# Kernel optimization log

Hardware: AMD Instinct MI355X
Metric: run time of the kernel (lower is better)

The kernel has to match this reference:

```python
import jax, jax.numpy as jnp
import numpy as np

IN_DIM, H_DIM, Y_DIM, ROLLOUT = 1024, 2048, 1024, 512


def setup_inputs() -> dict:
    key = jax.random.key(0)
    ks = jax.random.split(key, 4)
    return {
        "x": jax.random.normal(ks[0], (1, ROLLOUT, IN_DIM), dtype=jnp.float32),
        "h": jnp.zeros((H_DIM,), dtype=jnp.float32),
        "Wc": jax.random.normal(ks[1], (IN_DIM + H_DIM, H_DIM), dtype=jnp.float32) * 0.01,
        "Wu": jax.random.normal(ks[2], (IN_DIM + H_DIM, H_DIM), dtype=jnp.float32) * 0.01,
        "bc": jnp.zeros((H_DIM,), dtype=jnp.float32),
        "bu": jnp.zeros((H_DIM,), dtype=jnp.float32),
        "Wh_y": jax.random.normal(ks[3], (H_DIM, Y_DIM), dtype=jnp.float32) * 0.01,
        "by": jnp.zeros((Y_DIM,), dtype=jnp.float32),
    }


def reference(x, h, Wc, Wu, bc, bu, Wh_y, by):
    # x: [1, T, in_dim]; h: [h_dim]. Strict sequential GRU-style cell via scan.
    def step(h_prev, xt):
        xc = jnp.concatenate([xt, h_prev])           # [in+h]
        Lu = jax.nn.sigmoid(xc @ Wu + bu)            # update gate
        c_tilda = jnp.tanh(xc @ Wc + bc)             # candidate
        h_new = Lu * c_tilda + (1.0 - Lu) * h_prev
        y = h_new @ Wh_y + by
        return h_new, y

    h_final, ys = jax.lax.scan(step, h, x[0])        # ys: [T, y_dim]
    return ys, h_final
```

## Files before the change

### kernel.cpp

```cpp
#include <hip/hip_runtime.h>
#include <hip/hip_bf16.h>
#include <math.h>

#define T_STEPS 512
#define IN_DIM  1024
#define H_DIM   2048
#define Y_DIM   1024
#define NBLK    256
#define BTHREADS 512
#define NGRP    8
#define GRP_SZ  (NBLK / NGRP)

static __device__ __forceinline__ unsigned short f2bf(float f) {
    unsigned u = __float_as_uint(f);
    unsigned r = (u + 0x7FFFu + ((u >> 16) & 1u)) >> 16;
    return (unsigned short)r;
}

#define TM 64
#define TN 64
#define TK 16

__global__ __launch_bounds__(256) void gemm_bias(
    const float* __restrict__ A, const float* __restrict__ B,
    const float* __restrict__ bias, float* __restrict__ C,
    int M, int N, int K, int lda, int ldb, int ldc)
{
    __shared__ float As[TK][TM + 4];
    __shared__ float Bs[TK][TN + 4];

    const int n0 = blockIdx.x * TN;
    const int m0 = blockIdx.y * TM;
    const int tid = threadIdx.x;
    const int tx = tid & 15;
    const int ty = tid >> 4;

    float acc[4][4] = {};

    for (int k0 = 0; k0 < K; k0 += TK) {
        #pragma unroll
        for (int l = tid; l < TM * TK; l += 256) {
            int tt = l >> 4, kk = l & 15;
            As[kk][tt] = A[(m0 + tt) * lda + (k0 + kk)];
        }
        #pragma unroll
        for (int l = tid; l < TK * TN; l += 256) {
            int kk = l >> 6, jj = l & 63;
            Bs[kk][jj] = B[(k0 + kk) * ldb + (n0 + jj)];
        }
        __syncthreads();
        #pragma unroll
        for (int kk = 0; kk < TK; ++kk) {
            float4 a = *(const float4*)&As[kk][ty * 4];
            float4 b = *(const float4*)&Bs[kk][tx * 4];
            acc[0][0] = fmaf(a.x, b.x, acc[0][0]);
            acc[0][1] = fmaf(a.x, b.y, acc[0][1]);
            acc[0][2] = fmaf(a.x, b.z, acc[0][2]);
            acc[0][3] = fmaf(a.x, b.w, acc[0][3]);
            acc[1][0] = fmaf(a.y, b.x, acc[1][0]);
            acc[1][1] = fmaf(a.y, b.y, acc[1][1]);
            acc[1][2] = fmaf(a.y, b.z, acc[1][2]);
            acc[1][3] = fmaf(a.y, b.w, acc[1][3]);
            acc[2][0] = fmaf(a.z, b.x, acc[2][0]);
            acc[2][1] = fmaf(a.z, b.y, acc[2][1]);
            acc[2][2] = fmaf(a.z, b.z, acc[2][2]);
            acc[2][3] = fmaf(a.z, b.w, acc[2][3]);
            acc[3][0] = fmaf(a.w, b.x, acc[3][0]);
            acc[3][1] = fmaf(a.w, b.y, acc[3][1]);
            acc[3][2] = fmaf(a.w, b.z, acc[3][2]);
            acc[3][3] = fmaf(a.w, b.w, acc[3][3]);
        }
        __syncthreads();
    }

    float4 bv = *(const float4*)&bias[n0 + tx * 4];
    #pragma unroll
    for (int r = 0; r < 4; ++r) {
        float4 o;
        o.x = acc[r][0] + bv.x;
        o.y = acc[r][1] + bv.y;
        o.z = acc[r][2] + bv.z;
        o.w = acc[r][3] + bv.w;
        *(float4*)&C[(m0 + ty * 4 + r) * ldc + (n0 + tx * 4)] = o;
    }
}

__global__ __launch_bounds__(BTHREADS) void gru_seq(
    const float* __restrict__ Wu_h,
    const float* __restrict__ Wc_h,
    const float* __restrict__ XU,
    const float* __restrict__ XC,
    const float* __restrict__ h0,
    float* __restrict__ H,
    unsigned* __restrict__ bar)
{
    __shared__ unsigned w_lds[2][8][H_DIM / 2];

    const int tid = threadIdx.x;
    const int jb = blockIdx.x * 8;

    for (int idx = tid; idx < 2 * 8 * (H_DIM / 2); idx += BTHREADS) {
        int m = idx >> 13;
        int r = idx & 8191;
        int w = r >> 10;
        int p = r & 1023;
        const float* W = m ? Wc_h : Wu_h;
        int j = jb + w;
        float v0 = W[(2 * p) * H_DIM + j];
        float v1 = W[(2 * p + 1) * H_DIM + j];
        w_lds[m][w][p] = (unsigned)f2bf(v0) | ((unsigned)f2bf(v1) << 16);
    }
    __syncthreads();

    const int w = tid >> 6;
    const int lane = tid & 63;
    const int j = jb + w;
    const unsigned* __restrict__ wu = w_lds[0][w];
    const unsigned* __restrict__ wc = w_lds[1][w];

    unsigned* grp  = bar + (blockIdx.x & (NGRP - 1)) * 64;
    unsigned* root = bar + 512;

    for (int t = 0; t < T_STEPS; ++t) {
        float xu = 0.f, xc = 0.f;
        if (lane == 0) {
            xu = XU[t * H_DIM + j];
            xc = XC[t * H_DIM + j];
        }

        if (t > 0 && tid == 0) {
            unsigned tgt = (unsigned)t * NGRP;
            while (__hip_atomic_load(root, __ATOMIC_RELAXED, __HIP_MEMORY_SCOPE_AGENT) < tgt) {
                __builtin_amdgcn_s_sleep(8);
            }
        }
        __syncthreads();

        const float* hsrc = t ? (H + (t - 1) * H_DIM) : h0;
        const unsigned long long* h64 = (const unsigned long long*)hsrc;

        float hp = 0.f;
        if (lane == 0) {
            hp = __hip_atomic_load((const float*)hsrc + j,
                                   __ATOMIC_RELAXED, __HIP_MEMORY_SCOPE_AGENT);
        }

        float au = 0.f, ac = 0.f;
        #pragma unroll
        for (int i = 0; i < 16; ++i) {
            int p = i * 64 + lane;
            unsigned long long v = __hip_atomic_load(h64 + p,
                                       __ATOMIC_RELAXED, __HIP_MEMORY_SCOPE_AGENT);
            float hx = __uint_as_float((unsigned)v);
            float hy = __uint_as_float((unsigned)(v >> 32));
            unsigned pu = wu[p];
            unsigned pc = wc[p];
            float u0 = __uint_as_float(pu << 16);
            float u1 = __uint_as_float(pu & 0xFFFF0000u);
            float c0 = __uint_as_float(pc << 16);
            float c1 = __uint_as_float(pc & 0xFFFF0000u);
            au = fmaf(hx, u0, au);
            au = fmaf(hy, u1, au);
            ac = fmaf(hx, c0, ac);
            ac = fmaf(hy, c1, ac);
        }
        #pragma unroll
        for (int off = 32; off; off >>= 1) {
            au += __shfl_down(au, off);
            ac += __shfl_down(ac, off);
        }
        if (lane == 0) {
            float pre_u = au + xu;
            float pre_c = ac + xc;
            float ug = 1.f / (1.f + expf(-pre_u));
            float cg = tanhf(pre_c);
            float hnew = ug * cg + (1.f - ug) * hp;
            __hip_atomic_store(H + t * H_DIM + j, hnew,
                               __ATOMIC_RELAXED, __HIP_MEMORY_SCOPE_AGENT);
        }

        asm volatile("s_waitcnt vmcnt(0)" ::: "memory");
        __syncthreads();
        if (tid == 0 && t < T_STEPS - 1) {
            unsigned old = __hip_atomic_fetch_add(grp, 1u,
                               __ATOMIC_RELAXED, __HIP_MEMORY_SCOPE_AGENT);
            if (old == (unsigned)(t + 1) * GRP_SZ - 1u) {
                __hip_atomic_fetch_add(root, 1u,
                                       __ATOMIC_RELAXED, __HIP_MEMORY_SCOPE_AGENT);
            }
        }
    }
}

extern "C" void kernel_launch(void* const* d_in, const int* in_sizes, int n_in,
                              void* d_out, int out_size, void* d_ws, size_t ws_size,
                              hipStream_t stream)
{
    const float* x   = (const float*)d_in[0];
    const float* h0  = (const float*)d_in[1];
    const float* Wc  = (const float*)d_in[2];
    const float* Wu  = (const float*)d_in[3];
    const float* bc  = (const float*)d_in[4];
    const float* bu  = (const float*)d_in[5];
    const float* Why = (const float*)d_in[6];
    const float* by  = (const float*)d_in[7];
    float* out = (float*)d_out;

    float* ws = (float*)d_ws;
    float* XU = ws;
    float* XC = ws + (T_STEPS * H_DIM);
    float* H  = ws + 2 * (T_STEPS * H_DIM);
    unsigned* bar = (unsigned*)(ws + 3 * (T_STEPS * H_DIM));

    hipMemsetAsync(bar, 0, 4096, stream);

    gemm_bias<<<dim3(H_DIM / TN, T_STEPS / TM), 256, 0, stream>>>(
        x, Wu, bu, XU, T_STEPS, H_DIM, IN_DIM, IN_DIM, H_DIM, H_DIM);
    gemm_bias<<<dim3(H_DIM / TN, T_STEPS / TM), 256, 0, stream>>>(
        x, Wc, bc, XC, T_STEPS, H_DIM, IN_DIM, IN_DIM, H_DIM, H_DIM);

    gru_seq<<<NBLK, BTHREADS, 0, stream>>>(
        Wu + IN_DIM * H_DIM, Wc + IN_DIM * H_DIM, XU, XC, h0, H, bar);

    gemm_bias<<<dim3(Y_DIM / TN, T_STEPS / TM), 256, 0, stream>>>(
        H, Why, by, out, T_STEPS, Y_DIM, H_DIM, H_DIM, Y_DIM, Y_DIM);

    hipMemcpyAsync(out + T_STEPS * Y_DIM, H + (T_STEPS - 1) * H_DIM,
                   H_DIM * sizeof(float), hipMemcpyDeviceToDevice, stream);
}
```

Measured before the change: 2.741 ms.

## Halve GRU blocks, keep weights in registers, flatten grid barrier, widen GEMM tiles

The sequential GRU kernel now runs on 128 blocks, each handling 16 hidden units, with each wave computing two units. Recurrent weights are held in registers as packed bf16 rather than in LDS. The two-level group/root barrier is replaced by a single level: eight threads each poll one of eight group counters, with a shorter sleep. This removes the root-counter hop and LDS reads on the per-step critical path. The input and output GEMMs widen the N tile to 128 and use float4 loads. The cost is higher register pressure, 64 weight registers per thread, and more polling traffic.

New measurement: 4.200 ms. +53.3%, slower.

```diff
diff --git a/kernel.cpp b/kernel.cpp
--- a/kernel.cpp
+++ b/kernel.cpp
@@ -6,19 +6,22 @@
 #define IN_DIM  1024
 #define H_DIM   2048
 #define Y_DIM   1024
-#define NBLK    256
-#define BTHREADS 512
-#define NGRP    8
-#define GRP_SZ  (NBLK / NGRP)
+
+#define NBLK2   128
+#define BT2     512
+#define NLINE   8
+#define BLKS_PER_LINE (NBLK2 / NLINE)
 
 static __device__ __forceinline__ unsigned short f2bf(float f) {
     unsigned u = __float_as_uint(f);
     unsigned r = (u + 0x7FFFu + ((u >> 16) & 1u)) >> 16;
     return (unsigned short)r;
 }
+static __device__ __forceinline__ float bflo(unsigned p) { return __uint_as_float(p << 16); }
+static __device__ __forceinline__ float bfhi(unsigned p) { return __uint_as_float(p & 0xFFFF0000u); }
 
 #define TM 64
-#define TN 64
+#define TN 128
 #define TK 16
 
 __global__ __launch_bounds__(256) void gemm_bias(
@@ -35,57 +38,56 @@
     const int tx = tid & 15;
     const int ty = tid >> 4;
 
-    float acc[4][4] = {};
+    float acc[4][8] = {};
 
     for (int k0 = 0; k0 < K; k0 += TK) {
-        #pragma unroll
-        for (int l = tid; l < TM * TK; l += 256) {
-            int tt = l >> 4, kk = l & 15;
-            As[kk][tt] = A[(m0 + tt) * lda + (k0 + kk)];
-        }
-        #pragma unroll
-        for (int l = tid; l < TK * TN; l += 256) {
-            int kk = l >> 6, jj = l & 63;
-            Bs[kk][jj] = B[(k0 + kk) * ldb + (n0 + jj)];
+        {
+            int mm = tid & 63, kq = tid >> 6;
+            float4 a = *(const float4*)&A[(m0 + mm) * lda + k0 + 4 * kq];
+            As[4 * kq + 0][mm] = a.x;
+            As[4 * kq + 1][mm] = a.y;
+            As[4 * kq + 2][mm] = a.z;
+            As[4 * kq + 3][mm] = a.w;
+        }
+        #pragma unroll
+        for (int l = tid; l < 512; l += 256) {
+            int kk = l >> 5, jj = (l & 31) * 4;
+            *(float4*)&Bs[kk][jj] = *(const float4*)&B[(k0 + kk) * ldb + n0 + jj];
         }
         __syncthreads();
         #pragma unroll
         for (int kk = 0; kk < TK; ++kk) {
-            float4 a = *(const float4*)&As[kk][ty * 4];
-            float4 b = *(const float4*)&Bs[kk][tx * 4];
-            acc[0][0] = fmaf(a.x, b.x, acc[0][0]);
-            acc[0][1] = fmaf(a.x, b.y, acc[0][1]);
-            acc[0][2] = fmaf(a.x, b.z, acc[0][2]);
-            acc[0][3] = fmaf(a.x, b.w, acc[0][3]);
-            acc[1][0] = fmaf(a.y, b.x, acc[1][0]);
-            acc[1][1] = fmaf(a.y, b.y, acc[1][1]);
-            acc[1][2] = fmaf(a.y, b.z, acc[1][2]);
-            acc[1][3] = fmaf(a.y, b.w, acc[1][3]);
-            acc[2][0] = fmaf(a.z, b.x, acc[2][0]);
-            acc[2][1] = fmaf(a.z, b.y, acc[2][1]);
-            acc[2][2] = fmaf(a.z, b.z, acc[2][2]);
-            acc[2][3] = fmaf(a.z, b.w, acc[2][3]);
-            acc[3][0] = fmaf(a.w, b.x, acc[3][0]);
-            acc[3][1] = fmaf(a.w, b.y, acc[3][1]);
-            acc[3][2] = fmaf(a.w, b.z, acc[3][2]);
-            acc[3][3] = fmaf(a.w, b.w, acc[3][3]);
+            float4 a  = *(const float4*)&As[kk][ty * 4];
+            float4 b0 = *(const float4*)&Bs[kk][tx * 8];
+            float4 b1 = *(const float4*)&Bs[kk][tx * 8 + 4];
+            const float av[4] = {a.x, a.y, a.z, a.w};
+            const float bv[8] = {b0.x, b0.y, b0.z, b0.w, b1.x, b1.y, b1.z, b1.w};
+            #pragma unroll
+            for (int r = 0; r < 4; ++r)
+                #pragma unroll
+                for (int c = 0; c < 8; ++c)
+                    acc[r][c] = fmaf(av[r], bv[c], acc[r][c]);
         }
         __syncthreads();
     }
 
-    float4 bv = *(const float4*)&bias[n0 + tx * 4];
+    float4 bv0 = *(const float4*)&bias[n0 + tx * 8];
+    float4 bv1 = *(const float4*)&bias[n0 + tx * 8 + 4];
+    const float bb[8] = {bv0.x, bv0.y, bv0.z, bv0.w, bv1.x, bv1.y, bv1.z, bv1.w};
     #pragma unroll
     for (int r = 0; r < 4; ++r) {
-        float4 o;
-        o.x = acc[r][0] + bv.x;
-        o.y = acc[r][1] + bv.y;
-        o.z = acc[r][2] + bv.z;
-        o.w = acc[r][3] + bv.w;
-        *(float4*)&C[(m0 + ty * 4 + r) * ldc + (n0 + tx * 4)] = o;
-    }
-}
-
-__global__ __launch_bounds__(BTHREADS) void gru_seq(
+        float4 o0, o1;
+        o0.x = acc[r][0] + bb[0]; o0.y = acc[r][1] + bb[1];
+        o0.z = acc[r][2] + bb[2]; o0.w = acc[r][3] + bb[3];
+        o1.x = acc[r][4] + bb[4]; o1.y = acc[r][5] + bb[5];
+        o1.z = acc[r][6] + bb[6]; o1.w = acc[r][7] + bb[7];
+        float* cp = &C[(m0 + ty * 4 + r) * ldc + n0 + tx * 8];
+        *(float4*)cp = o0;
+        *(float4*)(cp + 4) = o1;
+    }
+}
+
+__global__ __launch_bounds__(BT2) void gru_seq(
     const float* __restrict__ Wu_h,
     const float* __restrict__ Wc_h,
     const float* __restrict__ XU,
@@ -94,100 +96,102 @@
     float* __restrict__ H,
     unsigned* __restrict__ bar)
 {
-    __shared__ unsigned w_lds[2][8][H_DIM / 2];
-
-    const int tid = threadIdx.x;
-    const int jb = blockIdx.x * 8;
-
-    for (int idx = tid; idx < 2 * 8 * (H_DIM / 2); idx += BTHREADS) {
-        int m = idx >> 13;
-        int r = idx & 8191;
-        int w = r >> 10;
-        int p = r & 1023;
-        const float* W = m ? Wc_h : Wu_h;
-        int j = jb + w;
-        float v0 = W[(2 * p) * H_DIM + j];
-        float v1 = W[(2 * p + 1) * H_DIM + j];
-        w_lds[m][w][p] = (unsigned)f2bf(v0) | ((unsigned)f2bf(v1) << 16);
-    }
-    __syncthreads();
-
-    const int w = tid >> 6;
+    const int tid  = threadIdx.x;
+    const int w    = tid >> 6;
     const int lane = tid & 63;
-    const int j = jb + w;
-    const unsigned* __restrict__ wu = w_lds[0][w];
-    const unsigned* __restrict__ wc = w_lds[1][w];
-
-    unsigned* grp  = bar + (blockIdx.x & (NGRP - 1)) * 64;
-    unsigned* root = bar + 512;
+    const int jb   = blockIdx.x * 16;
+    const int j0   = jb + 2 * w;
+
+    unsigned wr[4][16];
+    {
+        const float* Wm[2] = {Wu_h, Wc_h};
+        #pragma unroll
+        for (int m = 0; m < 2; ++m) {
+            #pragma unroll
+            for (int c = 0; c < 2; ++c) {
+                const float* Wp = Wm[m] + j0 + c;
+                #pragma unroll
+                for (int i = 0; i < 16; ++i) {
+                    int p = i * 64 + lane;
+                    float v0 = Wp[(size_t)(2 * p) * H_DIM];
+                    float v1 = Wp[(size_t)(2 * p + 1) * H_DIM];
+                    wr[2 * m + c][i] = (unsigned)f2bf(v0) | ((unsigned)f2bf(v1) << 16);
+                }
+            }
+        }
+    }
+
+    unsigned* mygrp = bar + (blockIdx.x & (NLINE - 1)) * 64;
 
     for (int t = 0; t < T_STEPS; ++t) {
-        float xu = 0.f, xc = 0.f;
+        float2 xu = make_float2(0.f, 0.f), xc = make_float2(0.f, 0.f);
         if (lane == 0) {
-            xu = XU[t * H_DIM + j];
-            xc = XC[t * H_DIM + j];
-        }
-
-        if (t > 0 && tid == 0) {
-            unsigned tgt = (unsigned)t * NGRP;
-            while (__hip_atomic_load(root, __ATOMIC_RELAXED, __HIP_MEMORY_SCOPE_AGENT) < tgt) {
-                __builtin_amdgcn_s_sleep(8);
+            xu = *(const float2*)(XU + (size_t)t * H_DIM + j0);
+            xc = *(const float2*)(XC + (size_t)t * H_DIM + j0);
+        }
+
+        if (t > 0) {
+            if (tid < NLINE) {
+                unsigned tgt = (unsigned)t * BLKS_PER_LINE;
+                while (__hip_atomic_load(bar + tid * 64, __ATOMIC_RELAXED,
+                                         __HIP_MEMORY_SCOPE_AGENT) < tgt) {
+                    __builtin_amdgcn_s_sleep(1);
+                }
             }
-        }
-        __syncthreads();
-
-        const float* hsrc = t ? (H + (t - 1) * H_DIM) : h0;
+            __syncthreads();
+        }
+
+        const float* hsrc = t ? (H + (size_t)(t - 1) * H_DIM) : h0;
         const unsigned long long* h64 = (const unsigned long long*)hsrc;
 
-        float hp = 0.f;
+        float2 hp = make_float2(0.f, 0.f);
         if (lane == 0) {
-            hp = __hip_atomic_load((const float*)hsrc + j,
-                                   __ATOMIC_RELAXED, __HIP_MEMORY_SCOPE_AGENT);
-        }
-
-        float au = 0.f, ac = 0.f;
+            unsigned long long u = __hip_atomic_load(
+                (const unsigned long long*)(hsrc + j0),
+                __ATOMIC_RELAXED, __HIP_MEMORY_SCOPE_AGENT);
+            hp.x = __uint_as_float((unsigned)u);
+            hp.y = __uint_as_float((unsigned)(u >> 32));
+        }
+
+        float a0 = 0.f, a1 = 0.f, a2 = 0.f, a3 = 0.f;
         #pragma unroll
         for (int i = 0; i < 16; ++i) {
-            int p = i * 64 + lane;
-            unsigned long long v = __hip_atomic_load(h64 + p,
+            unsigned long long v = __hip_atomic_load(h64 + i * 64 + lane,
                                        __ATOMIC_RELAXED, __HIP_MEMORY_SCOPE_AGENT);
             float hx = __uint_as_float((unsigned)v);
             float hy = __uint_as_float((unsigned)(v >> 32));
-            unsigned pu = wu[p];
-            unsigned pc = wc[p];
-            float u0 = __uint_as_float(pu << 16);
-            float u1 = __uint_as_float(pu & 0xFFFF0000u);
-            float c0 = __uint_as_float(pc << 16);
-            float c1 = __uint_as_float(pc & 0xFFFF0000u);
-            au = fmaf(hx, u0, au);
-            au = fmaf(hy, u1, au);
-            ac = fmaf(hx, c0, ac);
-            ac = fmaf(hy, c1, ac);
+            unsigned pu0 = wr[0][i], pu1 = wr[1][i];
+            unsigned pc0 = wr[2][i], pc1 = wr[3][i];
+            a0 = fmaf(hx, bflo(pu0), a0); a0 = fmaf(hy, bfhi(pu0), a0);
+            a1 = fmaf(hx, bflo(pu1), a1); a1 = fmaf(hy, bfhi(pu1), a1);
+            a2 = fmaf(hx, bflo(pc0), a2); a2 = fmaf(hy, bfhi(pc0), a2);
+            a3 = fmaf(hx, bflo(pc1), a3); a3 = fmaf(hy, bfhi(pc1), a3);
         }
         #pragma unroll
         for (int off = 32; off; off >>= 1) {
-            au += __shfl_down(au, off);
-            ac += __shfl_down(ac, off);
+            a0 += __shfl_down(a0, off);
+            a1 += __shfl_down(a1, off);
+            a2 += __shfl_down(a2, off);
+            a3 += __shfl_down(a3, off);
         }
         if (lane == 0) {
-            float pre_u = au + xu;
-            float pre_c = ac + xc;
-            float ug = 1.f / (1.f + expf(-pre_u));
-            float cg = tanhf(pre_c);
-            float hnew = ug * cg + (1.f - ug) * hp;
-            __hip_atomic_store(H + t * H_DIM + j, hnew,
+            float u0 = 1.f / (1.f + expf(-(a0 + xu.x)));
+            float u1 = 1.f / (1.f + expf(-(a1 + xu.y)));
+            float c0 = tanhf(a2 + xc.x);
+            float c1 = tanhf(a3 + xc.y);
+            float hn0 = u0 * c0 + (1.f - u0) * hp.x;
+            float hn1 = u1 * c1 + (1.f - u1) * hp.y;
+            unsigned long long pv = (unsigned long long)__float_as_uint(hn0) |
+                                    ((unsigned long long)__float_as_uint(hn1) << 32);
+            __hip_atomic_store((unsigned long long*)(H + (size_t)t * H_DIM + j0), pv,
                                __ATOMIC_RELAXED, __HIP_MEMORY_SCOPE_AGENT);
         }
 
         asm volatile("s_waitcnt vmcnt(0)" ::: "memory");
         __syncthreads();
         if (tid == 0 && t < T_STEPS - 1) {
-            unsigned old = __hip_atomic_fetch_add(grp, 1u,
-                               __ATOMIC_RELAXED, __HIP_MEMORY_SCOPE_AGENT);
-            if (old == (unsigned)(t + 1) * GRP_SZ - 1u) {
-                __hip_atomic_fetch_add(root, 1u,
-                                       __ATOMIC_RELAXED, __HIP_MEMORY_SCOPE_AGENT);
-            }
+            __hip_atomic_fetch_add(mygrp, 1u,
+                                   __ATOMIC_RELAXED, __HIP_MEMORY_SCOPE_AGENT);
         }
     }
 }
@@ -219,7 +223,7 @@
     gemm_bias<<<dim3(H_DIM / TN, T_STEPS / TM), 256, 0, stream>>>(
         x, Wc, bc, XC, T_STEPS, H_DIM, IN_DIM, IN_DIM, H_DIM, H_DIM);
 
-    gru_seq<<<NBLK, BTHREADS, 0, stream>>>(
+    gru_seq<<<NBLK2, BT2, 0, stream>>>(
         Wu + IN_DIM * H_DIM, Wc + IN_DIM * H_DIM, XU, XC, h0, H, bar);
 
     gemm_bias<<<dim3(Y_DIM / TN, T_STEPS / TM), 256, 0, stream>>>(
```
